# Performance work log

Measured on AMD Instinct MI355X. Metric: run time of the kernel, lower is better.

The kernel has to match this reference:

```python
import jax, jax.numpy as jnp
import numpy as np

D_BINS = 88
DEPTH_MIN, DEPTH_MAX = 1.0, 45.0
BN_EPS = 1e-5


def setup_inputs() -> dict:
    key = jax.random.key(0)
    ks = jax.random.split(key, 8)
    N, C, H, W = 12, 256, 32, 88
    CC = 128  # context channels
    return {
        "x": jax.random.normal(ks[0], (N, C, H, W), dtype=jnp.float32),
        "dnet_w": jax.random.normal(ks[1], (D_BINS + CC, C), dtype=jnp.float32) * 0.05,
        "dnet_b": jax.random.normal(ks[2], (D_BINS + CC,), dtype=jnp.float32) * 0.05,
        "proj_w": jax.random.normal(ks[3], (C, CC), dtype=jnp.float32) * 0.05,
        "bn_gamma": jax.random.uniform(ks[4], (C,), dtype=jnp.float32) + 0.5,
        "bn_beta": jax.random.normal(ks[5], (C,), dtype=jnp.float32) * 0.1,
        "bn_mean": jax.random.normal(ks[6], (C,), dtype=jnp.float32) * 0.1,
        "bn_var": jax.random.uniform(ks[7], (C,), dtype=jnp.float32) + 0.5,
    }


def reference(x, dnet_w, dnet_b, proj_w, bn_gamma, bn_beta, bn_mean, bn_var):
    # depth_net: 1x1 conv == per-pixel matmul over channels
    dc = jnp.einsum('nchw,oc->nohw', x, dnet_w) + dnet_b[None, :, None, None]
    depth_logits = dc[:, :D_BINS]          # [N, D, H, W]
    tran_feat = dc[:, D_BINS:]             # [N, CC, H, W]
    # context_proj (1x1 conv, no bias) + BatchNorm2d (inference) + exact GELU
    tran_feat = jnp.einsum('nkhw,ck->nchw', tran_feat, proj_w)
    inv_std = jax.lax.rsqrt(bn_var + BN_EPS)
    tran_feat = (tran_feat - bn_mean[None, :, None, None]) * (bn_gamma * inv_std)[None, :, None, None] \
                + bn_beta[None, :, None, None]
    tran_feat = jax.nn.gelu(tran_feat, approximate=False)
    depth_prob = jax.nn.softmax(depth_logits, axis=1)  # [N, D, H, W]
    depth_values = jnp.linspace(DEPTH_MIN, DEPTH_MAX, D_BINS)
    depth_weight = depth_values / depth_values.mean()  # [D]
    # collapse_z=True: bev[n,c,h,w] = tran_feat[n,c,h,w] * sum_d depth_prob[n,d,h,w]*w[d]
    # (fused form of the [N,C,D,H,W] outer-product volume followed by sum over D)
    s = jnp.einsum('ndhw,d->nhw', depth_prob, depth_weight)  # [N, H, W]
    bev = tran_feat * s[:, None, :, :]
    return bev, depth_logits, depth_prob
```

## Files before the change

### kernel.cpp

```cpp
#include <hip/hip_runtime.h>
#include <hip/hip_bf16.h>
#include <math.h>

#define C_IN 256
#define CC 128
#define NDEPTH 88
#define HW 2816
#define NB 12
#define TILE 64
#define NTILES 44
#define LOG_OFF   ((size_t)8650752)
#define PROB_OFF  ((size_t)11624448)

typedef __attribute__((ext_vector_type(8))) short bf16x8;
typedef __attribute__((ext_vector_type(4))) float f32x4;

__device__ __forceinline__ unsigned short f2bf(float f) {
    unsigned int u = __float_as_uint(f);
    unsigned int r = (u + 0x7fffu + ((u >> 16) & 1u)) >> 16;
    return (unsigned short)r;
}
__device__ __forceinline__ unsigned int pack2(float a, float b) {
    return (unsigned int)f2bf(a) | ((unsigned int)f2bf(b) << 16);
}
__device__ __forceinline__ void bar_lgkm() {
    asm volatile("s_waitcnt lgkmcnt(0)\n\ts_barrier" ::: "memory");
}
__device__ __forceinline__ float gelu_fast(float v) {
    float u = v * (1.5957691216f + 0.07135481283f * v * v);
    return v / (1.f + __expf(-u));
}

__global__ void prep_kernel(const float* __restrict__ dnet_w,
                            const float* __restrict__ proj_w,
                            const float* __restrict__ gamma,
                            const float* __restrict__ beta,
                            const float* __restrict__ mean,
                            const float* __restrict__ var,
                            uint4* __restrict__ w1df,
                            uint4* __restrict__ w1tf,
                            uint4* __restrict__ projf,
                            float* __restrict__ scale,
                            float* __restrict__ shift) {
    const int tid = blockIdx.x * blockDim.x + threadIdx.x;
    const int N1 = 48 * 64, N2 = 64 * 64, N3 = 64 * 64;
    for (int e = tid; e < N1 + N2 + N3; e += gridDim.x * blockDim.x) {
        uint4 v = {0u, 0u, 0u, 0u};
        if (e < N1) {
            const int fb = e >> 6, l = e & 63;
            const int kh = fb / 24, rem = fb % 24, ks = rem / 6, dt = rem % 6;
            const int m = l & 15, g = l >> 4;
            const int o = dt * 16 + m;
            if (o < NDEPTH) {
                const float* p = dnet_w + o * 256 + kh * 128 + ks * 32 + g * 8;
                v.x = pack2(p[0], p[1]); v.y = pack2(p[2], p[3]);
                v.z = pack2(p[4], p[5]); v.w = pack2(p[6], p[7]);
            }
            w1df[e] = v;
        } else if (e < N1 + N2) {
            const int e2 = e - N1;
            const int fb = e2 >> 6, l = e2 & 63;
            const int kh = fb / 32, rem = fb % 32, ks = rem / 8, tt = rem % 8;
            const int m = l & 15, g = l >> 4;
            const float* p = dnet_w + (NDEPTH + tt * 16 + m) * 256 + kh * 128 + ks * 32 + g * 8;
            v.x = pack2(p[0], p[1]); v.y = pack2(p[2], p[3]);
            v.z = pack2(p[4], p[5]); v.w = pack2(p[6], p[7]);
            w1tf[e2] = v;
        } else {
            const int e3 = e - N1 - N2;
            const int fb = e3 >> 6, l = e3 & 63;
            const int ks = fb >> 4, ct = fb & 15;
            const int m = l & 15, g = l >> 4;
            const float* p = proj_w + (ct * 16 + m) * 128 + ks * 32 + g * 8;
            v.x = pack2(p[0], p[1]); v.y = pack2(p[2], p[3]);
            v.z = pack2(p[4], p[5]); v.w = pack2(p[6], p[7]);
            projf[e3] = v;
        }
    }
    if (tid < 256) {
        float sc = gamma[tid] * rsqrtf(var[tid] + 1e-5f);
        scale[tid] = sc;
        shift[tid] = beta[tid] - mean[tid] * sc;
    }
}

__global__ __launch_bounds__(512, 4)
void fused_kernel(const float* __restrict__ x,
                  const float* __restrict__ dnet_b,
                  const uint4* __restrict__ w1df,
                  const uint4* __restrict__ w1tf,
                  const uint4* __restrict__ projf,
                  const float* __restrict__ scale,
                  const float* __restrict__ shift,
                  float* __restrict__ out) {
    __shared__ __align__(16) char buf[57344];
    __shared__ __align__(16) unsigned short trs[4][16 * 128];
    __shared__ float ss[4][16];
    __shared__ float biasd[96];
    __shared__ float biast[128];
    __shared__ float sc_s[256];
    __shared__ float sh_s[256];

    unsigned short* xs = (unsigned short*)buf;
    f32x4* partD = (f32x4*)buf;
    f32x4* partT = (f32x4*)(buf + 24576);

    const int bid = blockIdx.x;
    const int n   = bid / NTILES;
    const int hw0 = (bid % NTILES) * TILE;
    const int t     = threadIdx.x;
    const int lane  = t & 63;
    const int wv    = t >> 6;
    const int strip = wv & 3;
    const int khalf = wv >> 2;

    if (t < 96)       biasd[t] = (t < NDEPTH) ? dnet_b[t] : 0.f;
    else if (t < 224) biast[t - 96] = dnet_b[t - 8];
    if (t < 256) { sc_s[t] = scale[t]; sh_s[t] = shift[t]; }

    {
        const int hwl = t & 63;
        const int cg  = t >> 6;
        const float* xb = x + (size_t)n * C_IN * HW + hw0 + hwl;
        #pragma unroll
        for (int cb = 0; cb < 4; ++cb) {
            const int c0 = cb * 64 + cg * 8;
            float f[8];
            #pragma unroll
            for (int j = 0; j < 8; ++j) f[j] = xb[(size_t)(c0 + j) * HW];
            uint4 v;
            v.x = pack2(f[0], f[1]);
            v.y = pack2(f[2], f[3]);
            v.z = pack2(f[4], f[5]);
            v.w = pack2(f[6], f[7]);
            const int csw = (c0 >> 3) ^ (hwl & 7);
            *reinterpret_cast<uint4*>(&xs[hwl * 256 + csw * 8]) = v;
        }
    }
    bar_lgkm();

    const int g = lane >> 4;
    const int m = lane & 15;
    const int brow  = strip * 16 + m;
    const int hwcol = hw0 + strip * 16 + m;

    f32x4 accd[6], acct[8];
    #pragma unroll
    for (int i = 0; i < 6; ++i) accd[i] = (f32x4){0.f, 0.f, 0.f, 0.f};
    #pragma unroll
    for (int i = 0; i < 8; ++i) acct[i] = (f32x4){0.f, 0.f, 0.f, 0.f};
    {
        const bf16x8* w1dv = (const bf16x8*)w1df;
        const bf16x8* w1tv = (const bf16x8*)w1tf;
        #pragma unroll
        for (int ksl = 0; ksl < 4; ++ksl) {
            const int k0 = (khalf * 4 + ksl) * 32;
            const int csw = ((k0 >> 3) + g) ^ (brow & 7);
            bf16x8 b = *reinterpret_cast<const bf16x8*>(&xs[brow * 256 + csw * 8]);
            #pragma unroll
            for (int dt = 0; dt < 6; ++dt) {
                bf16x8 a = w1dv[((khalf * 4 + ksl) * 6 + dt) * 64 + lane];
                accd[dt] = __builtin_amdgcn_mfma_f32_16x16x32_bf16(a, b, accd[dt], 0, 0, 0);
            }
            #pragma unroll
            for (int tt = 0; tt < 8; ++tt) {
                bf16x8 a = w1tv[((khalf * 4 + ksl) * 8 + tt) * 64 + lane];
                acct[tt] = __builtin_amdgcn_mfma_f32_16x16x32_bf16(a, b, acct[tt], 0, 0, 0);
            }
        }
    }
    bar_lgkm();

    if (khalf == 0) {
        #pragma unroll
        for (int tt = 0; tt < 8; ++tt)
            partT[(strip * 8 + tt) * 64 + lane] = acct[tt];
    } else {
        #pragma unroll
        for (int dt = 0; dt < 6; ++dt)
            partD[(strip * 6 + dt) * 64 + lane] = accd[dt];
    }
    bar_lgkm();

    float mx = 0.f, inv = 0.f;
    if (khalf == 0) {
        #pragma unroll
        for (int dt = 0; dt < 6; ++dt) {
            accd[dt] += partD[(strip * 6 + dt) * 64 + lane];
            #pragma unroll
            for (int r = 0; r < 4; ++r)
                accd[dt][r] += biasd[dt * 16 + g * 4 + r];
        }
        mx = -1e30f;
        #pragma unroll
        for (int dt = 0; dt < 6; ++dt) {
            #pragma unroll
            for (int r = 0; r < 4; ++r) {
                const int o = dt * 16 + g * 4 + r;
                if (o < NDEPTH) mx = fmaxf(mx, accd[dt][r]);
            }
        }
        mx = fmaxf(mx, __shfl_xor(mx, 16));
        mx = fmaxf(mx, __shfl_xor(mx, 32));
        float sum = 0.f, spn = 0.f;
        #pragma unroll
        for (int dt = 0; dt < 6; ++dt) {
            #pragma unroll
            for (int r = 0; r < 4; ++r) {
                const int o = dt * 16 + g * 4 + r;
                if (o < NDEPTH) {
                    float e = __expf(accd[dt][r] - mx);
                    sum += e;
                    spn += e * ((1.f + (float)o * (44.f / 87.f)) * (1.f / 23.f));
                }
            }
        }
        sum += __shfl_xor(sum, 16);
        sum += __shfl_xor(sum, 32);
        spn += __shfl_xor(spn, 16);
        spn += __shfl_xor(spn, 32);
        inv = 1.0f / sum;
        if (lane < 16) ss[strip][m] = spn * inv;
    } else {
        #pragma unroll
        for (int tt = 0; tt < 8; ++tt)
            acct[tt] += partT[(strip * 8 + tt) * 64 + lane];
        unsigned short* tw = &trs[strip][0];
        #pragma unroll
        for (int tt = 0; tt < 8; ++tt) {
            const int cb = tt * 16 + g * 4;
            float v0 = acct[tt][0] + biast[cb + 0];
            float v1 = acct[tt][1] + biast[cb + 1];
            float v2 = acct[tt][2] + biast[cb + 2];
            float v3 = acct[tt][3] + biast[cb + 3];
            const int csw = (cb >> 3) ^ (m & 7);
            uint2 pkd;
            pkd.x = pack2(v0, v1);
            pkd.y = pack2(v2, v3);
            *reinterpret_cast<uint2*>(&tw[m * 128 + csw * 8 + (g & 1) * 4]) = pkd;
        }
    }
    bar_lgkm();

    const int ctb = khalf * 8;
    f32x4 acc2[8];
    #pragma unroll
    for (int i = 0; i < 8; ++i) acc2[i] = (f32x4){0.f, 0.f, 0.f, 0.f};
    {
        const bf16x8* pv = (const bf16x8*)projf;
        const unsigned short* tw = &trs[strip][0];
        #pragma unroll
        for (int ks = 0; ks < 4; ++ks) {
            const int k0 = ks * 32;
            const int csw = ((k0 >> 3) + g) ^ (m & 7);
            bf16x8 b = *reinterpret_cast<const bf16x8*>(&tw[m * 128 + csw * 8]);
            #pragma unroll
            for (int ct = 0; ct < 8; ++ct) {
                bf16x8 a = pv[(ks * 16 + ctb + ct) * 64 + lane];
                acc2[ct] = __builtin_amdgcn_mfma_f32_16x16x32_bf16(a, b, acc2[ct], 0, 0, 0);
            }
        }
    }

    {
        const float sp = ss[strip][m];
        float* bev = out + (size_t)n * C_IN * HW + hwcol;
        #pragma unroll
        for (int ct = 0; ct < 8; ++ct) {
            #pragma unroll
            for (int r = 0; r < 4; ++r) {
                const int cc = (ctb + ct) * 16 + g * 4 + r;
                float v  = acc2[ct][r] * sc_s[cc] + sh_s[cc];
                bev[(size_t)cc * HW] = gelu_fast(v) * sp;
            }
        }
    }

    if (khalf == 0) {
        float* lg = out + LOG_OFF  + (size_t)n * NDEPTH * HW + hwcol;
        float* pb = out + PROB_OFF + (size_t)n * NDEPTH * HW + hwcol;
        #pragma unroll
        for (int dt = 0; dt < 6; ++dt) {
            #pragma unroll
            for (int r = 0; r < 4; ++r) {
                const int o = dt * 16 + g * 4 + r;
                if (o < NDEPTH) {
                    lg[(size_t)o * HW] = accd[dt][r];
                    pb[(size_t)o * HW] = __expf(accd[dt][r] - mx) * inv;
                }
            }
        }
    }
}

extern "C" void kernel_launch(void* const* d_in, const int* in_sizes, int n_in,
                              void* d_out, int out_size, void* d_ws, size_t ws_size,
                              hipStream_t stream) {
    const float* x      = (const float*)d_in[0];
    const float* dnet_w = (const float*)d_in[1];
    const float* dnet_b = (const float*)d_in[2];
    const float* proj_w = (const float*)d_in[3];
    const float* gamma  = (const float*)d_in[4];
    const float* beta   = (const float*)d_in[5];
    const float* mean   = (const float*)d_in[6];
    const float* var    = (const float*)d_in[7];
    float* out = (float*)d_out;

    char* ws = (char*)d_ws;
    uint4* w1df = (uint4*)ws;
    uint4* w1tf = (uint4*)(ws + 49152);
    uint4* projf = (uint4*)(ws + 49152 + 65536);
    float* scale = (float*)(ws + 49152 + 65536 + 65536);
    float* shift = scale + 256;

    prep_kernel<<<96, 256, 0, stream>>>(dnet_w, proj_w, gamma, beta, mean, var,
                                        w1df, w1tf, projf, scale, shift);
    fused_kernel<<<NB * NTILES, 512, 0, stream>>>(x, dnet_b, w1df, w1tf, projf,
                                                  scale, shift, out);
}
```

Measured before the change: 129.0 us.

## Split depth and context GEMMs across waves, drop shared x staging

The fused kernel now uses 32-pixel tiles with 256-thread blocks. Within each strip, one wave computes the depth-logit GEMM plus softmax and the other computes the context GEMM. Each wave loads x directly from global memory into bf16 fragments, which removes the LDS staging of x, the K-split partial-sum exchange and two barriers, and cuts LDS use so more blocks fit per CU. The cost is that both waves of a strip read the same x values from global memory (duplicated loads served through cache), and each wave runs the full K=256 reduction, which lengthens its serial MFMA chain.

```diff
diff --git a/kernel.cpp b/kernel.cpp
--- a/kernel.cpp
+++ b/kernel.cpp
@@ -7,8 +7,8 @@
 #define NDEPTH 88
 #define HW 2816
 #define NB 12
-#define TILE 64
-#define NTILES 44
+#define TILE 32
+#define NTILES 88
 #define LOG_OFF   ((size_t)8650752)
 #define PROB_OFF  ((size_t)11624448)
 
@@ -22,6 +22,10 @@
 }
 __device__ __forceinline__ unsigned int pack2(float a, float b) {
     return (unsigned int)f2bf(a) | ((unsigned int)f2bf(b) << 16);
+}
+__device__ __forceinline__ short bfbits(float f) {
+    __hip_bfloat16 h = __float2bfloat16(f);
+    return *reinterpret_cast<short*>(&h);
 }
 __device__ __forceinline__ void bar_lgkm() {
     asm volatile("s_waitcnt lgkmcnt(0)\n\ts_barrier" ::: "memory");
@@ -48,11 +52,11 @@
         uint4 v = {0u, 0u, 0u, 0u};
         if (e < N1) {
             const int fb = e >> 6, l = e & 63;
-            const int kh = fb / 24, rem = fb % 24, ks = rem / 6, dt = rem % 6;
+            const int ks = fb / 6, dt = fb % 6;
             const int m = l & 15, g = l >> 4;
             const int o = dt * 16 + m;
             if (o < NDEPTH) {
-                const float* p = dnet_w + o * 256 + kh * 128 + ks * 32 + g * 8;
+                const float* p = dnet_w + o * 256 + ks * 32 + g * 8;
                 v.x = pack2(p[0], p[1]); v.y = pack2(p[2], p[3]);
                 v.z = pack2(p[4], p[5]); v.w = pack2(p[6], p[7]);
             }
@@ -60,9 +64,9 @@
         } else if (e < N1 + N2) {
             const int e2 = e - N1;
             const int fb = e2 >> 6, l = e2 & 63;
-            const int kh = fb / 32, rem = fb % 32, ks = rem / 8, tt = rem % 8;
+            const int ks = fb >> 3, tt = fb & 7;
             const int m = l & 15, g = l >> 4;
-            const float* p = dnet_w + (NDEPTH + tt * 16 + m) * 256 + kh * 128 + ks * 32 + g * 8;
+            const float* p = dnet_w + (NDEPTH + tt * 16 + m) * 256 + ks * 32 + g * 8;
             v.x = pack2(p[0], p[1]); v.y = pack2(p[2], p[3]);
             v.z = pack2(p[4], p[5]); v.w = pack2(p[6], p[7]);
             w1tf[e2] = v;
@@ -84,7 +88,7 @@
     }
 }
 
-__global__ __launch_bounds__(512, 4)
+__global__ __launch_bounds__(256, 6)
 void fused_kernel(const float* __restrict__ x,
                   const float* __restrict__ dnet_b,
                   const uint4* __restrict__ w1df,
@@ -93,17 +97,12 @@
                   const float* __restrict__ scale,
                   const float* __restrict__ shift,
                   float* __restrict__ out) {
-    __shared__ __align__(16) char buf[57344];
-    __shared__ __align__(16) unsigned short trs[4][16 * 128];
-    __shared__ float ss[4][16];
+    __shared__ __align__(16) unsigned short trs[2][16 * 128];
+    __shared__ float ss[2][16];
     __shared__ float biasd[96];
     __shared__ float biast[128];
     __shared__ float sc_s[256];
     __shared__ float sh_s[256];
-
-    unsigned short* xs = (unsigned short*)buf;
-    f32x4* partD = (f32x4*)buf;
-    f32x4* partT = (f32x4*)(buf + 24576);
 
     const int bid = blockIdx.x;
     const int n   = bid / NTILES;
@@ -111,87 +110,43 @@
     const int t     = threadIdx.x;
     const int lane  = t & 63;
     const int wv    = t >> 6;
-    const int strip = wv & 3;
-    const int khalf = wv >> 2;
+    const int strip = wv >> 1;
+    const int role  = wv & 1;
 
     if (t < 96)       biasd[t] = (t < NDEPTH) ? dnet_b[t] : 0.f;
     else if (t < 224) biast[t - 96] = dnet_b[t - 8];
-    if (t < 256) { sc_s[t] = scale[t]; sh_s[t] = shift[t]; }
-
-    {
-        const int hwl = t & 63;
-        const int cg  = t >> 6;
-        const float* xb = x + (size_t)n * C_IN * HW + hw0 + hwl;
-        #pragma unroll
-        for (int cb = 0; cb < 4; ++cb) {
-            const int c0 = cb * 64 + cg * 8;
-            float f[8];
-            #pragma unroll
-            for (int j = 0; j < 8; ++j) f[j] = xb[(size_t)(c0 + j) * HW];
-            uint4 v;
-            v.x = pack2(f[0], f[1]);
-            v.y = pack2(f[2], f[3]);
-            v.z = pack2(f[4], f[5]);
-            v.w = pack2(f[6], f[7]);
-            const int csw = (c0 >> 3) ^ (hwl & 7);
-            *reinterpret_cast<uint4*>(&xs[hwl * 256 + csw * 8]) = v;
-        }
-    }
-    bar_lgkm();
+    sc_s[t] = scale[t];
+    sh_s[t] = shift[t];
 
     const int g = lane >> 4;
     const int m = lane & 15;
-    const int brow  = strip * 16 + m;
     const int hwcol = hw0 + strip * 16 + m;
-
-    f32x4 accd[6], acct[8];
-    #pragma unroll
-    for (int i = 0; i < 6; ++i) accd[i] = (f32x4){0.f, 0.f, 0.f, 0.f};
-    #pragma unroll
-    for (int i = 0; i < 8; ++i) acct[i] = (f32x4){0.f, 0.f, 0.f, 0.f};
-    {
+    const float* xg = x + (size_t)n * C_IN * HW + hwcol;
+
+    if (role == 0) {
+        f32x4 accd[6];
+        #pragma unroll
+        for (int i = 0; i < 6; ++i) accd[i] = (f32x4){0.f, 0.f, 0.f, 0.f};
         const bf16x8* w1dv = (const bf16x8*)w1df;
-        const bf16x8* w1tv = (const bf16x8*)w1tf;
-        #pragma unroll
-        for (int ksl = 0; ksl < 4; ++ksl) {
-            const int k0 = (khalf * 4 + ksl) * 32;
-            const int csw = ((k0 >> 3) + g) ^ (brow & 7);
-            bf16x8 b = *reinterpret_cast<const bf16x8*>(&xs[brow * 256 + csw * 8]);
+        #pragma unroll
+        for (int ks = 0; ks < 8; ++ks) {
+            const int kb = ks * 32 + g * 8;
+            bf16x8 b;
+            #pragma unroll
+            for (int j = 0; j < 8; ++j) b[j] = bfbits(xg[(size_t)(kb + j) * HW]);
             #pragma unroll
             for (int dt = 0; dt < 6; ++dt) {
-                bf16x8 a = w1dv[((khalf * 4 + ksl) * 6 + dt) * 64 + lane];
+                bf16x8 a = w1dv[(ks * 6 + dt) * 64 + lane];
                 accd[dt] = __builtin_amdgcn_mfma_f32_16x16x32_bf16(a, b, accd[dt], 0, 0, 0);
             }
-            #pragma unroll
-            for (int tt = 0; tt < 8; ++tt) {
-                bf16x8 a = w1tv[((khalf * 4 + ksl) * 8 + tt) * 64 + lane];
-                acct[tt] = __builtin_amdgcn_mfma_f32_16x16x32_bf16(a, b, acct[tt], 0, 0, 0);
-            }
-        }
-    }
-    bar_lgkm();
-
-    if (khalf == 0) {
-        #pragma unroll
-        for (int tt = 0; tt < 8; ++tt)
-            partT[(strip * 8 + tt) * 64 + lane] = acct[tt];
-    } else {
-        #pragma unroll
-        for (int dt = 0; dt < 6; ++dt)
-            partD[(strip * 6 + dt) * 64 + lane] = accd[dt];
-    }
-    bar_lgkm();
-
-    float mx = 0.f, inv = 0.f;
-    if (khalf == 0) {
-        #pragma unroll
-        for (int dt = 0; dt < 6; ++dt) {
-            accd[dt] += partD[(strip * 6 + dt) * 64 + lane];
+        }
+        #pragma unroll
+        for (int dt = 0; dt < 6; ++dt) {
             #pragma unroll
             for (int r = 0; r < 4; ++r)
                 accd[dt][r] += biasd[dt * 16 + g * 4 + r];
         }
-        mx = -1e30f;
+        float mx = -1e30f;
         #pragma unroll
         for (int dt = 0; dt < 6; ++dt) {
             #pragma unroll
@@ -202,29 +157,55 @@
         }
         mx = fmaxf(mx, __shfl_xor(mx, 16));
         mx = fmaxf(mx, __shfl_xor(mx, 32));
+        float ev[6][4];
         float sum = 0.f, spn = 0.f;
         #pragma unroll
         for (int dt = 0; dt < 6; ++dt) {
             #pragma unroll
             for (int r = 0; r < 4; ++r) {
                 const int o = dt * 16 + g * 4 + r;
-                if (o < NDEPTH) {
-                    float e = __expf(accd[dt][r] - mx);
-                    sum += e;
-                    spn += e * ((1.f + (float)o * (44.f / 87.f)) * (1.f / 23.f));
-                }
+                float e = (o < NDEPTH) ? __expf(accd[dt][r] - mx) : 0.f;
+                ev[dt][r] = e;
+                sum += e;
+                spn += e * ((1.f + (float)o * (44.f / 87.f)) * (1.f / 23.f));
             }
         }
         sum += __shfl_xor(sum, 16);
         sum += __shfl_xor(sum, 32);
         spn += __shfl_xor(spn, 16);
         spn += __shfl_xor(spn, 32);
-        inv = 1.0f / sum;
+        const float inv = 1.0f / sum;
         if (lane < 16) ss[strip][m] = spn * inv;
+        float* lg = out + LOG_OFF  + (size_t)n * NDEPTH * HW + hwcol;
+        float* pb = out + PROB_OFF + (size_t)n * NDEPTH * HW + hwcol;
+        #pragma unroll
+        for (int dt = 0; dt < 6; ++dt) {
+            #pragma unroll
+            for (int r = 0; r < 4; ++r) {
+                const int o = dt * 16 + g * 4 + r;
+                if (o < NDEPTH) {
+                    lg[(size_t)o * HW] = accd[dt][r];
+                    pb[(size_t)o * HW] = ev[dt][r] * inv;
+                }
+            }
+        }
     } else {
-        #pragma unroll
-        for (int tt = 0; tt < 8; ++tt)
-            acct[tt] += partT[(strip * 8 + tt) * 64 + lane];
+        f32x4 acct[8];
+        #pragma unroll
+        for (int i = 0; i < 8; ++i) acct[i] = (f32x4){0.f, 0.f, 0.f, 0.f};
+        const bf16x8* w1tv = (const bf16x8*)w1tf;
+        #pragma unroll
+        for (int ks = 0; ks < 8; ++ks) {
+            const int kb = ks * 32 + g * 8;
+            bf16x8 b;
+            #pragma unroll
+            for (int j = 0; j < 8; ++j) b[j] = bfbits(xg[(size_t)(kb + j) * HW]);
+            #pragma unroll
+            for (int tt = 0; tt < 8; ++tt) {
+                bf16x8 a = w1tv[(ks * 8 + tt) * 64 + lane];
+                acct[tt] = __builtin_amdgcn_mfma_f32_16x16x32_bf16(a, b, acct[tt], 0, 0, 0);
+            }
+        }
         unsigned short* tw = &trs[strip][0];
         #pragma unroll
         for (int tt = 0; tt < 8; ++tt) {
@@ -242,7 +223,7 @@
     }
     bar_lgkm();
 
-    const int ctb = khalf * 8;
+    const int ctb = role * 8;
     f32x4 acc2[8];
     #pragma unroll
     for (int i = 0; i < 8; ++i) acc2[i] = (f32x4){0.f, 0.f, 0.f, 0.f};
@@ -272,22 +253,6 @@
                 const int cc = (ctb + ct) * 16 + g * 4 + r;
                 float v  = acc2[ct][r] * sc_s[cc] + sh_s[cc];
                 bev[(size_t)cc * HW] = gelu_fast(v) * sp;
-            }
-        }
-    }
-
-    if (khalf == 0) {
-        float* lg = out + LOG_OFF  + (size_t)n * NDEPTH * HW + hwcol;
-        float* pb = out + PROB_OFF + (size_t)n * NDEPTH * HW + hwcol;
-        #pragma unroll
-        for (int dt = 0; dt < 6; ++dt) {
-            #pragma unroll
-            for (int r = 0; r < 4; ++r) {
-                const int o = dt * 16 + g * 4 + r;
-                if (o < NDEPTH) {
-                    lg[(size_t)o * HW] = accd[dt][r];
-                    pb[(size_t)o * HW] = __expf(accd[dt][r] - mx) * inv;
-                }
             }
         }
     }
@@ -313,8 +278,8 @@
     float* scale = (float*)(ws + 49152 + 65536 + 65536);
     float* shift = scale + 256;
 
-    prep_kernel<<<96, 256, 0, stream>>>(dnet_w, proj_w, gamma, beta, mean, var,
-                                        w1df, w1tf, projf, scale, shift);
-    fused_kernel<<<NB * NTILES, 512, 0, stream>>>(x, dnet_b, w1df, w1tf, projf,
+    prep_kernel<<<176, 256, 0, stream>>>(dnet_w, proj_w, gamma, beta, mean, var,
+                                         w1df, w1tf, projf, scale, shift);
+    fused_kernel<<<NB * NTILES, 256, 0, stream>>>(x, dnet_b, w1df, w1tf, projf,
                                                   scale, shift, out);
 }
```

Result: slower. 132.2 us (+2.5%).
